# Kernel tuning notes

Measured on AMD Instinct MI355X. Metric: run time of the kernel, lower is better.

## Reference

```python
import jax, jax.numpy as jnp
import numpy as np

KS = 9            # kernel_size (odd)
SMOOTH_NR = 0.0
SMOOTH_DR = 1e-05
NDIM = 3


def _box1d(x, axis, k):
    """Same-padded running-window sum of width k along `axis` (ones-kernel conv).
    Uses a cumulative sum (integral image along one axis): O(1) per element."""
    pad = k // 2
    pw = [(0, 0)] * x.ndim
    pw[axis] = (pad, pad)
    xp = jnp.pad(x, pw)                      # zero-pad like F.conv with padding=k//2
    c = jnp.cumsum(xp, axis=axis)
    zshape = list(c.shape)
    zshape[axis] = 1
    c0 = jnp.concatenate([jnp.zeros(zshape, c.dtype), c], axis=axis)  # prefix sums with leading 0
    n = c0.shape[axis]
    upper = jax.lax.slice_in_dim(c0, k, n, axis=axis)
    lower = jax.lax.slice_in_dim(c0, 0, n - k, axis=axis)
    return upper - lower


def _box_sum(x, k):
    # Separable ones-kernel conv over all spatial axes (axes 2..ndim-1 of NC... layout)
    for ax in range(2, x.ndim):
        x = _box1d(x, ax, k)
    return x


def setup_inputs() -> dict:
    key = jax.random.key(0)
    k1, k2 = jax.random.split(key)
    shape = (2, 1, 160, 160, 160)
    pred = jax.random.normal(k1, shape, dtype=jnp.float32)
    target = jax.random.normal(k2, shape, dtype=jnp.float32)
    return {"pred": pred, "target": target}


def reference(pred, target):
    kvol = jnp.asarray(KS ** NDIM, dtype=pred.dtype)
    t_sum = _box_sum(target, KS)
    p_sum = _box_sum(pred, KS)
    t2_sum = _box_sum(target * target, KS)
    p2_sum = _box_sum(pred * pred, KS)
    tp_sum = _box_sum(target * pred, KS)
    t_avg = t_sum / kvol
    p_avg = p_sum / kvol
    cross = tp_sum - p_avg * t_sum
    t_var = t2_sum - t_avg * t_sum
    p_var = p2_sum - p_avg * p_sum
    ncc = (cross * cross + SMOOTH_NR) / (t_var * p_var + SMOOTH_DR)
    return -jnp.mean(ncc)
```

## Files before the change

kernel.cpp:

```cpp
#include <hip/hip_runtime.h>


typedef float v2f __attribute__((ext_vector_type(2)));
typedef float v4f __attribute__((ext_vector_type(4)));

#define TX 16
#define TY 16
#define ZC 40
#define PH 24
#define PW 24
#define XFP 16
#define NSTEP 48
#define NN 160
#define NPLANE (160*160)

__global__ void ncc_zero_ws(float* ws) { ws[0] = 0.0f; }

__global__ __launch_bounds__(256)
void ncc_fused(const float* __restrict__ pred, const float* __restrict__ target,
               float* __restrict__ ws) {
  __shared__ v2f st[PH * PW];
  __shared__ v4f xf4[PH * XFP];
  __shared__ float xf1[PH * XFP];
  __shared__ float wsum[4];

  const int tid = threadIdx.x;
  const int tx = tid & 15;
  const int ty = tid >> 4;

  int b = blockIdx.x;
  const int xt = b % 10; b /= 10;
  const int yt = b % 10; b /= 10;
  const int zc = b % 4;  b /= 4;
  const int x0 = xt * TX, y0 = yt * TY, z0 = zc * ZC;
  const size_t bbase = (size_t)b * (size_t)NN * (size_t)NPLANE;

  int soff0, soff1, soff2;
  bool sv0, sv1, sv2;
  {
    const int yy = tid / PW, xx = tid - yy * PW;
    const int gy = y0 + yy - 4, gx = x0 + xx - 4;
    sv0 = ((unsigned)gy < NN) && ((unsigned)gx < NN);
    soff0 = gy * NN + gx;
  }
  {
    const int pos = tid + 256;
    const int yy = pos / PW, xx = pos - yy * PW;
    const int gy = y0 + yy - 4, gx = x0 + xx - 4;
    sv1 = ((unsigned)gy < NN) && ((unsigned)gx < NN);
    soff1 = gy * NN + gx;
  }
  {
    const int pos = tid + 512;
    const int yy = pos / PW, xx = pos - yy * PW;
    const int gy = y0 + yy - 4, gx = x0 + xx - 4;
    sv2 = (tid < 64) && ((unsigned)gy < NN) && ((unsigned)gx < NN);
    soff2 = gy * NN + gx;
  }

  float rt0, rp0, rt1, rp1, rt2, rp2;

#define PRELOAD(SS) do {                                                      \
    const int zi_ = z0 - 4 + (SS);                                            \
    if ((unsigned)zi_ < NN) {                                                 \
      const size_t zb_ = bbase + (size_t)zi_ * (size_t)NPLANE;                \
      rt0 = sv0 ? target[zb_ + soff0] : 0.0f;                                 \
      rp0 = sv0 ? pred[zb_ + soff0]   : 0.0f;                                 \
      rt1 = sv1 ? target[zb_ + soff1] : 0.0f;                                 \
      rp1 = sv1 ? pred[zb_ + soff1]   : 0.0f;                                 \
      rt2 = sv2 ? target[zb_ + soff2] : 0.0f;                                 \
      rp2 = sv2 ? pred[zb_ + soff2]   : 0.0f;                                 \
    }                                                                         \
  } while (0)

#define XFOUT(YY, XX) do {                                                    \
    v2f m01 = {0.0f, 0.0f};                                                   \
    v2f m23 = {0.0f, 0.0f};                                                   \
    float s_tp = 0.0f;                                                        \
    _Pragma("unroll")                                                         \
    for (int dx = 0; dx < 9; ++dx) {                                          \
      const v2f v = st[(YY) * PW + (XX) + dx];                                \
      m01 += v;                                                               \
      m23 = __builtin_elementwise_fma(v, v, m23);                             \
      s_tp = fmaf(v.x, v.y, s_tp);                                            \
    }                                                                         \
    v4f o_; o_.x = m01.x; o_.y = m01.y; o_.z = m23.x; o_.w = m23.y;           \
    xf4[(YY) * XFP + (XX)] = o_;                                              \
    xf1[(YY) * XFP + (XX)] = s_tp;                                            \
  } while (0)

  v2f b01[9], b23[9];
  float b4[9];
  v2f run01 = {0.0f, 0.0f}, run23 = {0.0f, 0.0f};
  float run4 = 0.0f;
  #pragma unroll
  for (int j = 0; j < 9; ++j) {
    b01[j] = (v2f){0.0f, 0.0f}; b23[j] = (v2f){0.0f, 0.0f}; b4[j] = 0.0f;
  }
  float acc = 0.0f;
  const float inv_kvol = 1.0f / 729.0f;

#define ZBODY(PP) do {                                                        \
    const int s = s0 + (PP);                                                  \
    if (s < NSTEP) {                                                          \
      const int zi = z0 - 4 + s;                                              \
      const bool zvalid = ((unsigned)zi < NN);             \
      v2f c01 = {0.0f, 0.0f}, c23 = {0.0f, 0.0f};                             \
      float c4 = 0.0f;                                                        \
      if (zvalid) {                                                           \
        v2f w_;                                                               \
        w_.x = rt0; w_.y = rp0; st[tid] = w_;                                 \
        w_.x = rt1; w_.y = rp1; st[tid + 256] = w_;                           \
        if (tid < 64) { w_.x = rt2; w_.y = rp2; st[tid + 512] = w_; }         \
        __syncthreads();                                   \
        for (int pos = tid; pos < PH * TX; pos += 256) {                      \
          const int yy = pos >> 4;                                            \
          const int xx = pos & 15;                                            \
          XFOUT(yy, xx);                                                      \
        }                                                                     \
        __syncthreads();                    \
      }                                                                       \
              \
      if (s + 1 < NSTEP) { PRELOAD(s + 1); }                                  \
      if (zvalid) {                                                           \
        v4f a4 = {0.0f, 0.0f, 0.0f, 0.0f};                                    \
        _Pragma("unroll")                                                     \
        for (int dy = 0; dy < 9; ++dy) {                                      \
          a4 += xf4[(ty + dy) * XFP + tx];               \
          c4 += xf1[(ty + dy) * XFP + tx];                                    \
        }                                                                     \
        c01.x = a4.x; c01.y = a4.y; c23.x = a4.z; c23.y = a4.w;               \
      }                                                                       \
      run01 += c01 - b01[(PP)]; b01[(PP)] = c01;                              \
      run23 += c23 - b23[(PP)]; b23[(PP)] = c23;                              \
      run4  += c4  - b4[(PP)];  b4[(PP)]  = c4;                               \
      if (s >= 8) {                                                           \
        const v2f avg = run01 * inv_kvol;                                     \
        const v2f var = __builtin_elementwise_fma(-avg, run01, run23);        \
        const float cross = fmaf(-avg.y, run01.x, run4);                      \
        acc += (cross * cross) / (var.x * var.y + 1e-5f);                     \
      }                                                                       \
    }                                                                         \
  } while (0)

  PRELOAD(0);

  for (int s0 = 0; s0 < NSTEP; s0 += 9) {
    ZBODY(0); ZBODY(1); ZBODY(2); ZBODY(3); ZBODY(4);
    ZBODY(5); ZBODY(6); ZBODY(7); ZBODY(8);
  }
#undef ZBODY
#undef XFOUT
#undef PRELOAD

  #pragma unroll
  for (int off = 32; off > 0; off >>= 1)
    acc += __shfl_down(acc, off, 64);
  if ((tid & 63) == 0) wsum[tid >> 6] = acc;
  __syncthreads();
  if (tid == 0) {
    float tot = wsum[0] + wsum[1] + wsum[2] + wsum[3];
    atomicAdd(ws, tot);
  }
}

__global__ void ncc_finalize(const float* __restrict__ ws, float* __restrict__ out) {
  out[0] = -ws[0] * (1.0f / 8192000.0f);
}

extern "C" void kernel_launch(void* const* d_in, const int* in_sizes, int n_in,
                              void* d_out, int out_size, void* d_ws, size_t ws_size,
                              hipStream_t stream) {
  const float* pred   = (const float*)d_in[0];
  const float* target = (const float*)d_in[1];
  float* out = (float*)d_out;
  float* ws  = (float*)d_ws;

  ncc_zero_ws<<<1, 1, 0, stream>>>(ws);
  ncc_fused<<<800, 256, 0, stream>>>(pred, target, ws);
  ncc_finalize<<<1, 1, 0, stream>>>(ws, out);
}
```

Baseline: 78.52 us.

## Use running y-window sums in shared memory and pipeline z consumption by one step

The y-direction box sum is now computed by 128 threads, each producing two adjacent output rows with a sliding window, instead of every thread summing 9 rows. Results go to a double-buffered shared array that the z-accumulation reads one step later. This lets the y pass of plane s overlap the z update of plane s-1 without an extra barrier. It cuts shared-memory reads in the y pass but leaves half the threads idle in that phase, adds shared memory and buffer management, and adds one extra pipeline step at the end.

```diff
diff --git a/kernel.cpp b/kernel.cpp
--- a/kernel.cpp
+++ b/kernel.cpp
@@ -22,6 +22,8 @@
   __shared__ v2f st[PH * PW];
   __shared__ v4f xf4[PH * XFP];
   __shared__ float xf1[PH * XFP];
+  __shared__ v4f yf4[2][TY * TX];
+  __shared__ float yf1[2][TY * TX];
   __shared__ float wsum[4];
 
   const int tid = threadIdx.x;
@@ -100,54 +102,81 @@
   float acc = 0.0f;
   const float inv_kvol = 1.0f / 729.0f;
 
-#define ZBODY(PP) do {                                                        \
+#define ZBODY(PP, CSLOT) do {                                                 \
     const int s = s0 + (PP);                                                  \
-    if (s < NSTEP) {                                                          \
-      const int zi = z0 - 4 + s;                                              \
-      const bool zvalid = ((unsigned)zi < NN);             \
-      v2f c01 = {0.0f, 0.0f}, c23 = {0.0f, 0.0f};                             \
-      float c4 = 0.0f;                                                        \
-      if (zvalid) {                                                           \
-        v2f w_;                                                               \
-        w_.x = rt0; w_.y = rp0; st[tid] = w_;                                 \
-        w_.x = rt1; w_.y = rp1; st[tid + 256] = w_;                           \
-        if (tid < 64) { w_.x = rt2; w_.y = rp2; st[tid + 512] = w_; }         \
-        __syncthreads();                                   \
-        for (int pos = tid; pos < PH * TX; pos += 256) {                      \
-          const int yy = pos >> 4;                                            \
-          const int xx = pos & 15;                                            \
-          XFOUT(yy, xx);                                                      \
+    const bool zvS = (s < NSTEP) && ((unsigned)(z0 - 4 + s) < NN);            \
+    if (zvS) {                                                                \
+      v2f w_;                                                                 \
+      w_.x = rt0; w_.y = rp0; st[tid] = w_;                                   \
+      w_.x = rt1; w_.y = rp1; st[tid + 256] = w_;                             \
+      if (tid < 64) { w_.x = rt2; w_.y = rp2; st[tid + 512] = w_; }           \
+    }                                                                         \
+    __syncthreads();                       \
+    if (zvS) {                                                                \
+      for (int pos = tid; pos < PH * TX; pos += 256) {                        \
+        const int yy = pos >> 4;                                              \
+        const int xx = pos & 15;                                              \
+        XFOUT(yy, xx);                                                        \
+      }                                                                       \
+    }                                                                         \
+    __syncthreads();        \
+    if (s + 1 < NSTEP) { PRELOAD(s + 1); }                                    \
+    if (zvS && tid < 128) {                                                   \
+                      \
+      const int col = tid & 15;                                               \
+      const int r0  = (tid >> 4) * 2;                                         \
+      v4f* ya_ = yf4[s & 1];                                                  \
+      float* yb_ = yf1[s & 1];                                                \
+      v4f t0 = xf4[r0 * XFP + col];                                           \
+      float t01 = xf1[r0 * XFP + col];                                        \
+      v4f w = t0;                                                             \
+      float w1 = t01;                                                         \
+      _Pragma("unroll")                                                       \
+      for (int k = 1; k < 9; ++k) {                                           \
+        w += xf4[(r0 + k) * XFP + col];                                       \
+        w1 += xf1[(r0 + k) * XFP + col];                                      \
+      }                                                                       \
+      ya_[r0 * TX + col] = w;                                                 \
+      yb_[r0 * TX + col] = w1;                                                \
+      w  += xf4[(r0 + 9) * XFP + col] - t0;                                   \
+      w1 += xf1[(r0 + 9) * XFP + col] - t01;                                  \
+      ya_[(r0 + 1) * TX + col] = w;                                           \
+      yb_[(r0 + 1) * TX + col] = w1;                                          \
+    }                                                                         \
+       \
+    {                                                                         \
+      const int sm1 = s - 1;                                                  \
+      if (sm1 >= 0 && sm1 < NSTEP) {                                          \
+        const bool zvm1 = ((unsigned)(z0 - 4 + sm1) < NN);                    \
+        v2f c01 = {0.0f, 0.0f}, c23 = {0.0f, 0.0f};                           \
+        float c4 = 0.0f;                                                      \
+        if (zvm1) {                                                           \
+          const v4f a = yf4[(s & 1) ^ 1][ty * TX + tx];                       \
+          c4 = yf1[(s & 1) ^ 1][ty * TX + tx];                                \
+          c01.x = a.x; c01.y = a.y; c23.x = a.z; c23.y = a.w;                 \
         }                                                                     \
-        __syncthreads();                    \
+        run01 += c01 - b01[(CSLOT)]; b01[(CSLOT)] = c01;                      \
+        run23 += c23 - b23[(CSLOT)]; b23[(CSLOT)] = c23;                      \
+        run4  += c4  - b4[(CSLOT)];  b4[(CSLOT)]  = c4;                       \
+        if (sm1 >= 8) {                                                       \
+          const v2f avg = run01 * inv_kvol;                                   \
+          const v2f var = __builtin_elementwise_fma(-avg, run01, run23);      \
+          const float cross = fmaf(-avg.y, run01.x, run4);                    \
+          acc += (cross * cross) / (var.x * var.y + 1e-5f);                   \
+        }                                                                     \
       }                                                                       \
-              \
-      if (s + 1 < NSTEP) { PRELOAD(s + 1); }                                  \
-      if (zvalid) {                                                           \
-        v4f a4 = {0.0f, 0.0f, 0.0f, 0.0f};                                    \
-        _Pragma("unroll")                                                     \
-        for (int dy = 0; dy < 9; ++dy) {                                      \
-          a4 += xf4[(ty + dy) * XFP + tx];               \
-          c4 += xf1[(ty + dy) * XFP + tx];                                    \
-        }                                                                     \
-        c01.x = a4.x; c01.y = a4.y; c23.x = a4.z; c23.y = a4.w;               \
-      }                                                                       \
-      run01 += c01 - b01[(PP)]; b01[(PP)] = c01;                              \
-      run23 += c23 - b23[(PP)]; b23[(PP)] = c23;                              \
-      run4  += c4  - b4[(PP)];  b4[(PP)]  = c4;                               \
-      if (s >= 8) {                                                           \
-        const v2f avg = run01 * inv_kvol;                                     \
-        const v2f var = __builtin_elementwise_fma(-avg, run01, run23);        \
-        const float cross = fmaf(-avg.y, run01.x, run4);                      \
-        acc += (cross * cross) / (var.x * var.y + 1e-5f);                     \
-      }                                                                       \
     }                                                                         \
   } while (0)
 
   PRELOAD(0);
 
-  for (int s0 = 0; s0 < NSTEP; s0 += 9) {
-    ZBODY(0); ZBODY(1); ZBODY(2); ZBODY(3); ZBODY(4);
-    ZBODY(5); ZBODY(6); ZBODY(7); ZBODY(8);
+  for (int s0 = 0; s0 < 45; s0 += 9) {
+    ZBODY(0, 8); ZBODY(1, 0); ZBODY(2, 1); ZBODY(3, 2); ZBODY(4, 3);
+    ZBODY(5, 4); ZBODY(6, 5); ZBODY(7, 6); ZBODY(8, 7);
+  }
+  {
+    const int s0 = 45;
+    ZBODY(0, 8); ZBODY(1, 0); ZBODY(2, 1); ZBODY(3, 2);
   }
 #undef ZBODY
 #undef XFOUT
```

Result: slower. 102.3 us (+30.3%).

## Vectorize halo loads as float2 and compute two x-outputs per thread with running sum

Applied to the files above, without the earlier changes.

Global halo loads now fetch two adjacent x elements per thread as float2, which cuts the number of load instructions per plane. The shared staging tile is padded to a pitch of 25 to avoid LDS bank conflicts. The x-pass now has 192 threads each produce two adjacent outputs, the second one updated from the first by a sliding add/subtract. This replaces the strided loop that ran 384 outputs over 256 threads and cuts the x-direction LDS reads. In exchange the pair-aligned validity check assumes even tile edges, and the sliding update changes the floating-point summation order slightly.

```diff
diff --git a/kernel.cpp b/kernel.cpp
--- a/kernel.cpp
+++ b/kernel.cpp
@@ -9,6 +9,7 @@
 #define ZC 40
 #define PH 24
 #define PW 24
+#define PWP 25
 #define XFP 16
 #define NSTEP 48
 #define NN 160
@@ -19,7 +20,7 @@
 __global__ __launch_bounds__(256)
 void ncc_fused(const float* __restrict__ pred, const float* __restrict__ target,
                float* __restrict__ ws) {
-  __shared__ v2f st[PH * PW];
+  __shared__ v2f st[PH * PWP];
   __shared__ v4f xf4[PH * XFP];
   __shared__ float xf1[PH * XFP];
   __shared__ float wsum[4];
@@ -35,58 +36,48 @@
   const int x0 = xt * TX, y0 = yt * TY, z0 = zc * ZC;
   const size_t bbase = (size_t)b * (size_t)NN * (size_t)NPLANE;
 
-  int soff0, soff1, soff2;
-  bool sv0, sv1, sv2;
+  int poff0, poff1;
+  int pst0, pst1;
+  bool pv0, pv1;
   {
-    const int yy = tid / PW, xx = tid - yy * PW;
-    const int gy = y0 + yy - 4, gx = x0 + xx - 4;
-    sv0 = ((unsigned)gy < NN) && ((unsigned)gx < NN);
-    soff0 = gy * NN + gx;
+    const int row = tid / 12, cp = tid - row * 12;
+    const int gy = y0 + row - 4, gx = x0 + 2 * cp - 4;
+    pv0 = ((unsigned)gy < NN) && (gx >= 0) && (gx <= NN - 2);
+    poff0 = gy * NN + gx;
+    pst0 = row * PWP + 2 * cp;
   }
   {
-    const int pos = tid + 256;
-    const int yy = pos / PW, xx = pos - yy * PW;
-    const int gy = y0 + yy - 4, gx = x0 + xx - 4;
-    sv1 = ((unsigned)gy < NN) && ((unsigned)gx < NN);
-    soff1 = gy * NN + gx;
-  }
-  {
-    const int pos = tid + 512;
-    const int yy = pos / PW, xx = pos - yy * PW;
-    const int gy = y0 + yy - 4, gx = x0 + xx - 4;
-    sv2 = (tid < 64) && ((unsigned)gy < NN) && ((unsigned)gx < NN);
-    soff2 = gy * NN + gx;
+    const int i = tid + 256;
+    const int row = i / 12, cp = i - row * 12;
+    const int gy = y0 + row - 4, gx = x0 + 2 * cp - 4;
+    pv1 = (tid < 32) && ((unsigned)gy < NN) && (gx >= 0) && (gx <= NN - 2);
+    poff1 = gy * NN + gx;
+    pst1 = row * PWP + 2 * cp;
   }
 
-  float rt0, rp0, rt1, rp1, rt2, rp2;
+  const int xf_g   = tid / 24;
+  const int xf_row = tid - xf_g * 24;
+  const int xf_rd  = xf_row * PWP + 2 * xf_g;
+  const int xf_wr  = xf_row * XFP + 2 * xf_g;
+
+  float rt0, rp0, rt1, rp1;
+  float rt2, rp2, rt3, rp3;
 
 #define PRELOAD(SS) do {                                                      \
     const int zi_ = z0 - 4 + (SS);                                            \
     if ((unsigned)zi_ < NN) {                                                 \
       const size_t zb_ = bbase + (size_t)zi_ * (size_t)NPLANE;                \
-      rt0 = sv0 ? target[zb_ + soff0] : 0.0f;                                 \
-      rp0 = sv0 ? pred[zb_ + soff0]   : 0.0f;                                 \
-      rt1 = sv1 ? target[zb_ + soff1] : 0.0f;                                 \
-      rp1 = sv1 ? pred[zb_ + soff1]   : 0.0f;                                 \
-      rt2 = sv2 ? target[zb_ + soff2] : 0.0f;                                 \
-      rp2 = sv2 ? pred[zb_ + soff2]   : 0.0f;                                 \
+      if (pv0) {                                                              \
+        const float2 t2_ = *(const float2*)(target + zb_ + poff0);            \
+        const float2 p2_ = *(const float2*)(pred   + zb_ + poff0);            \
+        rt0 = t2_.x; rt1 = t2_.y; rp0 = p2_.x; rp1 = p2_.y;                   \
+      } else { rt0 = 0; rt1 = 0; rp0 = 0; rp1 = 0; }                          \
+      if (pv1) {                                                              \
+        const float2 t2_ = *(const float2*)(target + zb_ + poff1);            \
+        const float2 p2_ = *(const float2*)(pred   + zb_ + poff1);            \
+        rt2 = t2_.x; rt3 = t2_.y; rp2 = p2_.x; rp3 = p2_.y;                   \
+      } else { rt2 = 0; rt3 = 0; rp2 = 0; rp3 = 0; }                          \
     }                                                                         \
-  } while (0)
-
-#define XFOUT(YY, XX) do {                                                    \
-    v2f m01 = {0.0f, 0.0f};                                                   \
-    v2f m23 = {0.0f, 0.0f};                                                   \
-    float s_tp = 0.0f;                                                        \
-    _Pragma("unroll")                                                         \
-    for (int dx = 0; dx < 9; ++dx) {                                          \
-      const v2f v = st[(YY) * PW + (XX) + dx];                                \
-      m01 += v;                                                               \
-      m23 = __builtin_elementwise_fma(v, v, m23);                             \
-      s_tp = fmaf(v.x, v.y, s_tp);                                            \
-    }                                                                         \
-    v4f o_; o_.x = m01.x; o_.y = m01.y; o_.z = m23.x; o_.w = m23.y;           \
-    xf4[(YY) * XFP + (XX)] = o_;                                              \
-    xf1[(YY) * XFP + (XX)] = s_tp;                                            \
   } while (0)
 
   v2f b01[9], b23[9];
@@ -109,14 +100,38 @@
       float c4 = 0.0f;                                                        \
       if (zvalid) {                                                           \
         v2f w_;                                                               \
-        w_.x = rt0; w_.y = rp0; st[tid] = w_;                                 \
-        w_.x = rt1; w_.y = rp1; st[tid + 256] = w_;                           \
-        if (tid < 64) { w_.x = rt2; w_.y = rp2; st[tid + 512] = w_; }         \
+        w_.x = rt0; w_.y = rp0; st[pst0] = w_;                                \
+        w_.x = rt1; w_.y = rp1; st[pst0 + 1] = w_;                            \
+        if (tid < 32) {                                                       \
+          w_.x = rt2; w_.y = rp2; st[pst1] = w_;                              \
+          w_.x = rt3; w_.y = rp3; st[pst1 + 1] = w_;                          \
+        }                                                                     \
         __syncthreads();                                   \
-        for (int pos = tid; pos < PH * TX; pos += 256) {                      \
-          const int yy = pos >> 4;                                            \
-          const int xx = pos & 15;                                            \
-          XFOUT(yy, xx);                                                      \
+        if (tid < 192) {                                                      \
+            \
+          v2f m01 = {0.0f, 0.0f};                                             \
+          v2f m23 = {0.0f, 0.0f};                                             \
+          float s_tp = 0.0f;                                                  \
+          _Pragma("unroll")                                                   \
+          for (int k = 0; k < 9; ++k) {                                       \
+            const v2f v = st[xf_rd + k];                                      \
+            m01 += v;                                                         \
+            m23 = __builtin_elementwise_fma(v, v, m23);                       \
+            s_tp = fmaf(v.x, v.y, s_tp);                                      \
+          }                                                                   \
+          v4f o_; o_.x = m01.x; o_.y = m01.y; o_.z = m23.x; o_.w = m23.y;     \
+          xf4[xf_wr] = o_;                                                    \
+          xf1[xf_wr] = s_tp;                                                  \
+          const v2f vo = st[xf_rd];                                           \
+          const v2f vn = st[xf_rd + 9];                                       \
+          m01 += vn - vo;                                                     \
+          m23 = __builtin_elementwise_fma(vn, vn, m23);                       \
+          m23 = __builtin_elementwise_fma(-vo, vo, m23);                      \
+          s_tp = fmaf(vn.x, vn.y, s_tp);                                      \
+          s_tp = fmaf(-vo.x, vo.y, s_tp);                                     \
+          o_.x = m01.x; o_.y = m01.y; o_.z = m23.x; o_.w = m23.y;             \
+          xf4[xf_wr + 1] = o_;                                                \
+          xf1[xf_wr + 1] = s_tp;                                              \
         }                                                                     \
         __syncthreads();                    \
       }                                                                       \
@@ -126,7 +141,7 @@
         v4f a4 = {0.0f, 0.0f, 0.0f, 0.0f};                                    \
         _Pragma("unroll")                                                     \
         for (int dy = 0; dy < 9; ++dy) {                                      \
-          a4 += xf4[(ty + dy) * XFP + tx];               \
+          a4 += xf4[(ty + dy) * XFP + tx];                                    \
           c4 += xf1[(ty + dy) * XFP + tx];                                    \
         }                                                                     \
         c01.x = a4.x; c01.y = a4.y; c23.x = a4.z; c23.y = a4.w;               \
@@ -150,7 +165,6 @@
     ZBODY(5); ZBODY(6); ZBODY(7); ZBODY(8);
   }
 #undef ZBODY
-#undef XFOUT
 #undef PRELOAD
 
   #pragma unroll
```

New measurement: 103.9 us. 1.32x slower.
